# Performance work log

Measured on AMD Instinct MI355X. Metric: run time of the kernel, lower is better.

## Reference

```python
import jax, jax.numpy as jnp
import numpy as np

B, T, S, H = 4, 128, 512, 512
LN_EPS = 1e-5


def setup_inputs() -> dict:
    key = jax.random.key(0)
    ks = jax.random.split(key, 10)
    query = jax.random.normal(ks[0], (B, T, H), dtype=jnp.float32)
    encoder_outputs = jax.random.normal(ks[1], (B, S, H), dtype=jnp.float32)
    src_lengths = jax.random.randint(ks[2], (B,), 1, S + 1, dtype=jnp.int32)
    # Parameters (nn.Linear stores weight as (out, in); we apply x @ W.T)
    W_h = jax.random.normal(ks[3], (H, H), dtype=jnp.float32) / np.sqrt(H)
    W_s = jax.random.normal(ks[4], (H, H), dtype=jnp.float32) / np.sqrt(H)
    v = jax.random.normal(ks[5], (H,), dtype=jnp.float32) * 0.01
    W_out = jax.random.normal(ks[6], (H, 2 * H), dtype=jnp.float32) / np.sqrt(2 * H)
    b_out = jnp.zeros((H,), dtype=jnp.float32)
    gamma = jnp.ones((H,), dtype=jnp.float32)
    beta = jnp.zeros((H,), dtype=jnp.float32)
    return {
        "query": query, "encoder_outputs": encoder_outputs, "src_lengths": src_lengths,
        "W_h": W_h, "W_s": W_s, "v": v, "W_out": W_out, "b_out": b_out,
        "gamma": gamma, "beta": beta,
    }


def reference(query, encoder_outputs, src_lengths, W_h, W_s, v, W_out, b_out, gamma, beta):
    # Project query and encoder states: (b,t,h) and (b,s,h)
    q_proj = jnp.einsum('bth,oh->bto', query, W_s)
    k_proj = jnp.einsum('bsh,oh->bso', encoder_outputs, W_h)
    # Additive score: tanh over broadcast-add, then dot with v -> (b,t,s)
    score = jnp.einsum('btsh,h->bts', jnp.tanh(q_proj[:, :, None, :] + k_proj[:, None, :, :]), v)
    # Mask padded source positions (src_idx >= length)
    pad = jnp.arange(S)[None, :] >= src_lengths[:, None]          # (b,s)
    score = jnp.where(pad[:, None, :], -jnp.inf, score)
    attn = jax.nn.softmax(score, axis=-1)                          # (b,t,s)
    context = jnp.einsum('bts,bsh->bth', attn, encoder_outputs)    # (b,t,h)
    cq = jnp.concatenate([context, query], axis=-1)                # (b,t,2h)
    out = jnp.tanh(jnp.einsum('btk,ok->bto', cq, W_out) + b_out)
    # LayerNorm over last dim
    mu = jnp.mean(out, axis=-1, keepdims=True)
    var = jnp.mean(jnp.square(out - mu), axis=-1, keepdims=True)
    return (out - mu) / jnp.sqrt(var + LN_EPS) * gamma + beta
```

## Files before the change

kernel.cpp:

```cpp
#include <hip/hip_runtime.h>
#include <hip/hip_bf16.h>
#include <math.h>

#define B 4
#define T 128
#define S 512
#define H 512
#define QK_SCALE 2.8853900817779268f

#if defined(__has_builtin)
#if __has_builtin(__builtin_amdgcn_exp2f)
#define EXP2F(x) __builtin_amdgcn_exp2f(x)
#else
#define EXP2F(x) __expf((x) * 0.6931471805599453f)
#endif
#else
#define EXP2F(x) __expf((x) * 0.6931471805599453f)
#endif

typedef __attribute__((ext_vector_type(8))) short bf16x8;
typedef __attribute__((ext_vector_type(4))) float f32x4;

__device__ __forceinline__ short f2b(float x) {
    unsigned int u = __float_as_uint(x);
    u += 0x7fffu + ((u >> 16) & 1u);
    return (short)(u >> 16);
}
__device__ __forceinline__ float fast_tanh(float x) {
    float e = __expf(2.0f * x);
    float r = __builtin_amdgcn_rcpf(e + 1.0f);
    return 1.0f - 2.0f * r;
}

__global__ __launch_bounds__(256) void cvt_all(
    const float* __restrict__ q, const float* __restrict__ Ws,
    const float* __restrict__ Wh, const float* __restrict__ Wo,
    const float* __restrict__ enc, const int* __restrict__ slen,
    short* __restrict__ qb, short* __restrict__ wsb, short* __restrict__ whb,
    short* __restrict__ wob, short* __restrict__ eb, short* __restrict__ encT) {
    const int bid = blockIdx.x;
    const int tid = threadIdx.x;
    if (bid >= 1152) {
        __shared__ short tb[32][33];
        const int bid2 = bid - 1152;
        const int b = bid2 >> 8, s0 = ((bid2 >> 4) & 15) * 32, h0 = (bid2 & 15) * 32;
        if (s0 >= slen[b]) return;
        const int r = tid >> 3, c = (tid & 7) * 4;
        float4 a = *(const float4*)&enc[((size_t)(b * S + s0 + r)) * H + h0 + c];
        tb[c + 0][r] = f2b(a.x); tb[c + 1][r] = f2b(a.y);
        tb[c + 2][r] = f2b(a.z); tb[c + 3][r] = f2b(a.w);
        __syncthreads();
        ushort4 o = make_ushort4((unsigned short)tb[r][c], (unsigned short)tb[r][c + 1],
                                 (unsigned short)tb[r][c + 2], (unsigned short)tb[r][c + 3]);
        *(ushort4*)&encT[((size_t)(b * H + h0 + r)) * S + s0 + c] = o;
        return;
    }
    size_t i = ((size_t)bid * 256 + tid) * 8;
    const float* src; short* dst; size_t off;
    if (i < 262144)        { src = q;   dst = qb;  off = i; }
    else if (i < 524288)   { src = Ws;  dst = wsb; off = i - 262144; }
    else if (i < 786432)   { src = Wh;  dst = whb; off = i - 524288; }
    else if (i < 1310720)  { src = Wo;  dst = wob; off = i - 786432; }
    else                   { src = enc; dst = eb;  off = i - 1310720; }
    float4 a = *(const float4*)(src + off);
    float4 b = *(const float4*)(src + off + 4);
    ushort4 o0 = make_ushort4((unsigned short)f2b(a.x), (unsigned short)f2b(a.y),
                              (unsigned short)f2b(a.z), (unsigned short)f2b(a.w));
    ushort4 o1 = make_ushort4((unsigned short)f2b(b.x), (unsigned short)f2b(b.y),
                              (unsigned short)f2b(b.z), (unsigned short)f2b(b.w));
    *(ushort4*)(dst + off) = o0;
    *(ushort4*)(dst + off + 4) = o1;
}

#define MFMA4(APTR0, APTR1, BPTR0, BPTR1, KOFF)                                  \
    {                                                                            \
        bf16x8 a0 = *(const bf16x8*)((APTR0) + (KOFF));                          \
        bf16x8 a1 = *(const bf16x8*)((APTR1) + (KOFF));                          \
        bf16x8 b0 = *(const bf16x8*)((BPTR0) + (KOFF));                          \
        bf16x8 b1 = *(const bf16x8*)((BPTR1) + (KOFF));                          \
        acc00 = __builtin_amdgcn_mfma_f32_16x16x32_bf16(a0, b0, acc00, 0, 0, 0); \
        acc01 = __builtin_amdgcn_mfma_f32_16x16x32_bf16(a0, b1, acc01, 0, 0, 0); \
        acc10 = __builtin_amdgcn_mfma_f32_16x16x32_bf16(a1, b0, acc10, 0, 0, 0); \
        acc11 = __builtin_amdgcn_mfma_f32_16x16x32_bf16(a1, b1, acc11, 0, 0, 0); \
    }

__global__ __launch_bounds__(64) void mfma_proj(
    const short* __restrict__ qb, const short* __restrict__ eb,
    const short* __restrict__ wsb, const short* __restrict__ whb,
    const int* __restrict__ slen, float* __restrict__ qe, float* __restrict__ ke) {
    const int lane = threadIdx.x;
    const int r = lane & 15, kb = lane >> 4;
    const int n0 = blockIdx.x * 32;
    const int m0 = blockIdx.y * 32;
    const short* A; const short* W; float* C;
    if (m0 < 512) { A = qb + (size_t)m0 * H; W = wsb; C = qe + (size_t)m0 * H; }
    else {
        const int row = m0 - 512;
        if ((row & 511) >= slen[row >> 9]) return;
        A = eb + (size_t)row * H; W = whb; C = ke + (size_t)row * H;
    }
    const short* a0p = A + (size_t)r * H + kb * 8;
    const short* a1p = a0p + 16 * H;
    const short* b0p = W + (size_t)(n0 + r) * H + kb * 8;
    const short* b1p = b0p + 16 * H;
    f32x4 acc00 = {0,0,0,0}, acc01 = {0,0,0,0}, acc10 = {0,0,0,0}, acc11 = {0,0,0,0};
#pragma unroll 4
    for (int k = 0; k < H; k += 32) MFMA4(a0p, a1p, b0p, b1p, k)
    const int cr = kb * 4, cc = r;
#pragma unroll
    for (int g = 0; g < 4; ++g) {
        C[(size_t)(cr + g) * H + n0 + cc]           = EXP2F(acc00[g] * QK_SCALE);
        C[(size_t)(cr + g) * H + n0 + 16 + cc]      = EXP2F(acc01[g] * QK_SCALE);
        C[(size_t)(16 + cr + g) * H + n0 + cc]      = EXP2F(acc10[g] * QK_SCALE);
        C[(size_t)(16 + cr + g) * H + n0 + 16 + cc] = EXP2F(acc11[g] * QK_SCALE);
    }
}

__global__ __launch_bounds__(64) void score_v4(
    const float* __restrict__ qe, const float* __restrict__ ke,
    const float* __restrict__ v, const int* __restrict__ slen,
    float* __restrict__ scoreh) {
    const int qt = blockIdx.z & 3;
    const int b = blockIdx.z >> 2;
    const int L = slen[b];
    const int sbase = blockIdx.x * 16;
    if (sbase >= L) return;
    const int tbase = blockIdx.y * 8;
    const int hbase = qt * 128;
    __shared__ __align__(16) float qs[8][132];
    __shared__ __align__(16) float ks[16][132];
    __shared__ __align__(16) float vsh[128];
    const int lane = threadIdx.x;
    {
        const int r = lane >> 3, c = (lane & 7) * 16;
        const float* qsrc = qe + (size_t)(b * T + tbase + r) * H + hbase + c;
        const float* k0src = ke + (size_t)(b * S + sbase + r) * H + hbase + c;
        const float* k1src = k0src + 8 * H;
#pragma unroll
        for (int j = 0; j < 4; ++j) {
            *(float4*)&qs[r][c + j * 4] = *(const float4*)(qsrc + j * 4);
            *(float4*)&ks[r][c + j * 4] = *(const float4*)(k0src + j * 4);
            *(float4*)&ks[8 + r][c + j * 4] = *(const float4*)(k1src + j * 4);
        }
        float2 vv = *(const float2*)&v[hbase + lane * 2];
        *(float2*)&vsh[lane * 2] = make_float2(-2.f * vv.x, -2.f * vv.y);
    }
    __syncthreads();
    const int t = lane >> 3, s0 = (lane & 7) * 2;
    const float* qrow = &qs[t][0];
    const float* k0r = &ks[s0][0];
    const float* k1r = &ks[s0 + 1][0];
    float a0 = 0.f, a1 = 0.f, c0 = 0.f, c1 = 0.f;
#pragma unroll 2
    for (int i = 0; i < 128; i += 4) {
        float4 q4 = *(const float4*)&qrow[i];
        float4 ka = *(const float4*)&k0r[i];
        float4 kb = *(const float4*)&k1r[i];
        float4 v4 = *(const float4*)&vsh[i];
        a0 = fmaf(v4.x, __builtin_amdgcn_rcpf(fmaf(q4.x, ka.x, 1.f)), a0);
        c0 = fmaf(v4.x, __builtin_amdgcn_rcpf(fmaf(q4.x, kb.x, 1.f)), c0);
        a1 = fmaf(v4.y, __builtin_amdgcn_rcpf(fmaf(q4.y, ka.y, 1.f)), a1);
        c1 = fmaf(v4.y, __builtin_amdgcn_rcpf(fmaf(q4.y, kb.y, 1.f)), c1);
        a0 = fmaf(v4.z, __builtin_amdgcn_rcpf(fmaf(q4.z, ka.z, 1.f)), a0);
        c0 = fmaf(v4.z, __builtin_amdgcn_rcpf(fmaf(q4.z, kb.z, 1.f)), c0);
        a1 = fmaf(v4.w, __builtin_amdgcn_rcpf(fmaf(q4.w, ka.w, 1.f)), a1);
        c1 = fmaf(v4.w, __builtin_amdgcn_rcpf(fmaf(q4.w, kb.w, 1.f)), c1);
    }
    *(float2*)&scoreh[((size_t)qt * (B * T) + b * T + tbase + t) * S + sbase + s0] =
        make_float2(a0 + a1, c0 + c1);
}

__global__ __launch_bounds__(256) void softmax_k(
    const float* __restrict__ scoreh, const int* __restrict__ slen,
    short* __restrict__ attnb) {
    __shared__ float red[8];
    const int row = blockIdx.x;
    const int L = slen[row >> 7];
    const int tid = threadIdx.x;
    const int lane = tid & 63, wv = tid >> 6;
    const size_t sl = (size_t)(B * T) * S;
    const float* p0 = scoreh + (size_t)row * S;
    float x0 = p0[tid] + p0[sl + tid] + p0[2 * sl + tid] + p0[3 * sl + tid];
    float x1 = p0[tid + 256] + p0[sl + tid + 256] + p0[2 * sl + tid + 256] +
               p0[3 * sl + tid + 256];
    if (tid >= L) x0 = -INFINITY;
    if (tid + 256 >= L) x1 = -INFINITY;
    float m = fmaxf(x0, x1);
#pragma unroll
    for (int off = 32; off > 0; off >>= 1) m = fmaxf(m, __shfl_xor(m, off));
    if (lane == 0) red[wv] = m;
    __syncthreads();
    m = fmaxf(fmaxf(red[0], red[1]), fmaxf(red[2], red[3]));
    float e0 = __expf(x0 - m);
    float e1 = __expf(x1 - m);
    float sm = e0 + e1;
#pragma unroll
    for (int off = 32; off > 0; off >>= 1) sm += __shfl_xor(sm, off);
    if (lane == 0) red[4 + wv] = sm;
    __syncthreads();
    float inv = 1.0f / (red[4] + red[5] + red[6] + red[7]);
    short* o = attnb + (size_t)row * S;
    o[tid] = f2b(e0 * inv);
    o[tid + 256] = f2b(e1 * inv);
}

__global__ __launch_bounds__(64) void mfma_ctx(
    const short* __restrict__ attnb, const short* __restrict__ encT,
    const int* __restrict__ slen, short* __restrict__ ctxb) {
    const int b = blockIdx.z;
    const int L = slen[b];
    const int Keff = min(S, (L + 31) & ~31);
    const int lane = threadIdx.x;
    const int r = lane & 15, kb = lane >> 4;
    const int m0 = blockIdx.y * 32;
    const int n0 = blockIdx.x * 32;
    const short* A = attnb + (size_t)(b * T + m0) * S;
    const short* Bp = encT + (size_t)b * H * S;
    const short* a0p = A + (size_t)r * S + kb * 8;
    const short* a1p = a0p + 16 * S;
    const short* b0p = Bp + (size_t)(n0 + r) * S + kb * 8;
    const short* b1p = b0p + 16 * S;
    f32x4 acc00 = {0,0,0,0}, acc01 = {0,0,0,0}, acc10 = {0,0,0,0}, acc11 = {0,0,0,0};
#pragma unroll 2
    for (int k = 0; k < Keff; k += 32) MFMA4(a0p, a1p, b0p, b1p, k)
    const int cr = kb * 4, cc = r;
#pragma unroll
    for (int g = 0; g < 4; ++g) {
        size_t row0 = (size_t)(b * T + m0 + cr + g) * H;
        size_t row1 = (size_t)(b * T + m0 + 16 + cr + g) * H;
        ctxb[row0 + n0 + cc]      = f2b(acc00[g]);
        ctxb[row0 + n0 + 16 + cc] = f2b(acc01[g]);
        ctxb[row1 + n0 + cc]      = f2b(acc10[g]);
        ctxb[row1 + n0 + 16 + cc] = f2b(acc11[g]);
    }
}

__global__ __launch_bounds__(64) void mfma_out(
    const short* __restrict__ ctxb, const short* __restrict__ qb,
    const short* __restrict__ wob, const float* __restrict__ bias,
    float* __restrict__ pre) {
    const int lane = threadIdx.x;
    const int r = lane & 15, kb = lane >> 4;
    const int m0 = blockIdx.y * 32, n0 = blockIdx.x * 32;
    f32x4 acc00 = {0,0,0,0}, acc01 = {0,0,0,0}, acc10 = {0,0,0,0}, acc11 = {0,0,0,0};
    const short* b0p = wob + (size_t)(n0 + r) * (2 * H) + kb * 8;
    const short* b1p = b0p + 16 * (2 * H);
    {
        const short* a0p = ctxb + (size_t)(m0 + r) * H + kb * 8;
        const short* a1p = a0p + 16 * H;
#pragma unroll 4
        for (int k = 0; k < H; k += 32) MFMA4(a0p, a1p, b0p, b1p, k)
    }
    {
        const short* a0p = qb + (size_t)(m0 + r) * H + kb * 8;
        const short* a1p = a0p + 16 * H;
        const short* c0p = b0p + H;
        const short* c1p = b1p + H;
#pragma unroll 4
        for (int k = 0; k < H; k += 32) MFMA4(a0p, a1p, c0p, c1p, k)
    }
    const int cr = kb * 4, cc = r;
    float bn0 = bias[n0 + cc], bn1 = bias[n0 + 16 + cc];
#pragma unroll
    for (int g = 0; g < 4; ++g) {
        size_t row0 = (size_t)(m0 + cr + g) * H;
        size_t row1 = (size_t)(m0 + 16 + cr + g) * H;
        pre[row0 + n0 + cc]      = fast_tanh(acc00[g] + bn0);
        pre[row0 + n0 + 16 + cc] = fast_tanh(acc01[g] + bn1);
        pre[row1 + n0 + cc]      = fast_tanh(acc10[g] + bn0);
        pre[row1 + n0 + 16 + cc] = fast_tanh(acc11[g] + bn1);
    }
}

__global__ __launch_bounds__(256) void ln_out(
    const float* __restrict__ X, const float* __restrict__ gamma,
    const float* __restrict__ beta, float* __restrict__ out) {
    __shared__ float red[8];
    const int r = blockIdx.x;
    const int tid = threadIdx.x;
    const int lane = tid & 63, wv = tid >> 6;
    const float* x = X + (size_t)r * H;
    float x0 = x[tid], x1 = x[tid + 256];
    float s = x0 + x1;
#pragma unroll
    for (int off = 32; off > 0; off >>= 1) s += __shfl_down(s, off);
    if (lane == 0) red[wv] = s;
    __syncthreads();
    float mu = (red[0] + red[1] + red[2] + red[3]) * (1.0f / H);
    float d0 = x0 - mu, d1 = x1 - mu;
    float vsum = d0 * d0 + d1 * d1;
#pragma unroll
    for (int off = 32; off > 0; off >>= 1) vsum += __shfl_down(vsum, off);
    if (lane == 0) red[4 + wv] = vsum;
    __syncthreads();
    float var = (red[4] + red[5] + red[6] + red[7]) * (1.0f / H);
    float inv = rsqrtf(var + 1e-5f);
    out[(size_t)r * H + tid] = d0 * inv * gamma[tid] + beta[tid];
    out[(size_t)r * H + tid + 256] = d1 * inv * gamma[tid + 256] + beta[tid + 256];
}

extern "C" void kernel_launch(void* const* d_in, const int* in_sizes, int n_in,
                              void* d_out, int out_size, void* d_ws, size_t ws_size,
                              hipStream_t stream) {
    const float* query = (const float*)d_in[0];
    const float* enc   = (const float*)d_in[1];
    const int*   slen  = (const int*)d_in[2];
    const float* W_h   = (const float*)d_in[3];
    const float* W_s   = (const float*)d_in[4];
    const float* v     = (const float*)d_in[5];
    const float* W_out = (const float*)d_in[6];
    const float* b_out = (const float*)d_in[7];
    const float* gamma = (const float*)d_in[8];
    const float* beta  = (const float*)d_in[9];
    float* out = (float*)d_out;

    char* base = (char*)d_ws;
    short* qb     = (short*)(base + 0);
    short* wsb    = (short*)(base + 524288);
    short* whb    = (short*)(base + 1048576);
    short* wob    = (short*)(base + 1572864);
    short* eb     = (short*)(base + 2621440);
    float* qe     = (float*)(base + 4718592);
    float* ke     = (float*)(base + 5767168);
    float* scoreh = (float*)(base + 9961472);
    short* attnb  = (short*)(base + 14155776);
    short* encT   = (short*)(base + 14680064);
    short* ctxb   = (short*)(base + 16777216);
    float* pre    = (float*)(base + 17301504);

    cvt_all<<<dim3(2176), dim3(256), 0, stream>>>(query, W_s, W_h, W_out, enc, slen,
                                                  qb, wsb, whb, wob, eb, encT);
    mfma_proj<<<dim3(16, 80), dim3(64), 0, stream>>>(qb, eb, wsb, whb, slen, qe, ke);
    score_v4<<<dim3(32, 16, 16), dim3(64), 0, stream>>>(qe, ke, v, slen, scoreh);
    softmax_k<<<dim3(B * T), dim3(256), 0, stream>>>(scoreh, slen, attnb);
    mfma_ctx<<<dim3(16, 4, 4), dim3(64), 0, stream>>>(attnb, encT, slen, ctxb);
    mfma_out<<<dim3(16, 16), dim3(64), 0, stream>>>(ctxb, qb, wob, b_out, pre);
    ln_out<<<dim3(B * T), dim3(256), 0, stream>>>(pre, gamma, beta, out);
}
```

Baseline: 65.60 us.

## Fuse softmax, context GEMM, output GEMM and LayerNorm into one tail kernel

Replaces four launches (softmax, context MFMA, output MFMA, LayerNorm) with a single 1024-thread kernel per 16-row tile. Attention weights and context stay in shared memory, and LayerNorm statistics are reduced in-block with single-pass sum and sum-of-squares. This removes three launches and the global round trips for attn, ctx and pre. In exchange the tail runs on only 32 blocks, which limits parallelism, and each block re-reads the full W_out and encT slice. The context GEMM also drops the Keff length-based skip of padded positions.

```diff
diff --git a/kernel.cpp b/kernel.cpp
--- a/kernel.cpp
+++ b/kernel.cpp
@@ -170,133 +170,152 @@
         make_float2(a0 + a1, c0 + c1);
 }
 
-__global__ __launch_bounds__(256) void softmax_k(
+__global__ __launch_bounds__(1024) void tail_kernel(
     const float* __restrict__ scoreh, const int* __restrict__ slen,
-    short* __restrict__ attnb) {
-    __shared__ float red[8];
-    const int row = blockIdx.x;
-    const int L = slen[row >> 7];
+    const short* __restrict__ encT, const short* __restrict__ qb,
+    const short* __restrict__ wob, const float* __restrict__ bias,
+    const float* __restrict__ gamma, const float* __restrict__ beta,
+    float* __restrict__ out) {
+    __shared__ __align__(16) short attn_s[16][520];
+    __shared__ __align__(16) short ctx_s[16][520];
+    __shared__ float red_s[16][16];
+    __shared__ float red_q[16][16];
+    __shared__ float fin[16][2];
     const int tid = threadIdx.x;
-    const int lane = tid & 63, wv = tid >> 6;
-    const size_t sl = (size_t)(B * T) * S;
-    const float* p0 = scoreh + (size_t)row * S;
-    float x0 = p0[tid] + p0[sl + tid] + p0[2 * sl + tid] + p0[3 * sl + tid];
-    float x1 = p0[tid + 256] + p0[sl + tid + 256] + p0[2 * sl + tid + 256] +
-               p0[3 * sl + tid + 256];
-    if (tid >= L) x0 = -INFINITY;
-    if (tid + 256 >= L) x1 = -INFINITY;
-    float m = fmaxf(x0, x1);
-#pragma unroll
-    for (int off = 32; off > 0; off >>= 1) m = fmaxf(m, __shfl_xor(m, off));
-    if (lane == 0) red[wv] = m;
-    __syncthreads();
-    m = fmaxf(fmaxf(red[0], red[1]), fmaxf(red[2], red[3]));
-    float e0 = __expf(x0 - m);
-    float e1 = __expf(x1 - m);
-    float sm = e0 + e1;
-#pragma unroll
-    for (int off = 32; off > 0; off >>= 1) sm += __shfl_xor(sm, off);
-    if (lane == 0) red[4 + wv] = sm;
-    __syncthreads();
-    float inv = 1.0f / (red[4] + red[5] + red[6] + red[7]);
-    short* o = attnb + (size_t)row * S;
-    o[tid] = f2b(e0 * inv);
-    o[tid + 256] = f2b(e1 * inv);
-}
-
-__global__ __launch_bounds__(64) void mfma_ctx(
-    const short* __restrict__ attnb, const short* __restrict__ encT,
-    const int* __restrict__ slen, short* __restrict__ ctxb) {
-    const int b = blockIdx.z;
+    const int w = tid >> 6, lane = tid & 63;
+    const int b = blockIdx.x >> 3;
+    const int tb = (blockIdx.x & 7) * 16;
     const int L = slen[b];
-    const int Keff = min(S, (L + 31) & ~31);
-    const int lane = threadIdx.x;
+
+    {
+        const int grow = b * T + tb + w;
+        const size_t sl = (size_t)(B * T) * S;
+        const float* p = scoreh + (size_t)grow * S + lane * 8;
+        float x[8];
+#pragma unroll
+        for (int j = 0; j < 2; ++j) {
+            float4 q0 = *(const float4*)(p + j * 4);
+            float4 q1 = *(const float4*)(p + sl + j * 4);
+            float4 q2 = *(const float4*)(p + 2 * sl + j * 4);
+            float4 q3 = *(const float4*)(p + 3 * sl + j * 4);
+            x[j * 4 + 0] = q0.x + q1.x + q2.x + q3.x;
+            x[j * 4 + 1] = q0.y + q1.y + q2.y + q3.y;
+            x[j * 4 + 2] = q0.z + q1.z + q2.z + q3.z;
+            x[j * 4 + 3] = q0.w + q1.w + q2.w + q3.w;
+        }
+        const int cbase = lane * 8;
+#pragma unroll
+        for (int j = 0; j < 8; ++j)
+            if (cbase + j >= L) x[j] = -INFINITY;
+        float m = x[0];
+#pragma unroll
+        for (int j = 1; j < 8; ++j) m = fmaxf(m, x[j]);
+#pragma unroll
+        for (int off = 1; off < 64; off <<= 1) m = fmaxf(m, __shfl_xor(m, off));
+        float e[8], sm = 0.f;
+#pragma unroll
+        for (int j = 0; j < 8; ++j) { e[j] = __expf(x[j] - m); sm += e[j]; }
+#pragma unroll
+        for (int off = 1; off < 64; off <<= 1) sm += __shfl_xor(sm, off);
+        float inv = 1.0f / sm;
+        ushort4 u0 = make_ushort4((unsigned short)f2b(e[0] * inv), (unsigned short)f2b(e[1] * inv),
+                                  (unsigned short)f2b(e[2] * inv), (unsigned short)f2b(e[3] * inv));
+        ushort4 u1 = make_ushort4((unsigned short)f2b(e[4] * inv), (unsigned short)f2b(e[5] * inv),
+                                  (unsigned short)f2b(e[6] * inv), (unsigned short)f2b(e[7] * inv));
+        *(ushort4*)&attn_s[w][lane * 8]     = u0;
+        *(ushort4*)&attn_s[w][lane * 8 + 4] = u1;
+    }
+    __syncthreads();
+
     const int r = lane & 15, kb = lane >> 4;
-    const int m0 = blockIdx.y * 32;
-    const int n0 = blockIdx.x * 32;
-    const short* A = attnb + (size_t)(b * T + m0) * S;
-    const short* Bp = encT + (size_t)b * H * S;
-    const short* a0p = A + (size_t)r * S + kb * 8;
-    const short* a1p = a0p + 16 * S;
-    const short* b0p = Bp + (size_t)(n0 + r) * S + kb * 8;
-    const short* b1p = b0p + 16 * S;
-    f32x4 acc00 = {0,0,0,0}, acc01 = {0,0,0,0}, acc10 = {0,0,0,0}, acc11 = {0,0,0,0};
-#pragma unroll 2
-    for (int k = 0; k < Keff; k += 32) MFMA4(a0p, a1p, b0p, b1p, k)
-    const int cr = kb * 4, cc = r;
+    const int n0 = w * 32;
+    {
+        f32x4 cc0 = {0,0,0,0}, cc1 = {0,0,0,0};
+        const short* bp0 = encT + ((size_t)(b * H + n0 + r)) * S + kb * 8;
+        const short* bp1 = bp0 + (size_t)16 * S;
+#pragma unroll 4
+        for (int k = 0; k < S; k += 32) {
+            bf16x8 a = *(const bf16x8*)&attn_s[r][k + kb * 8];
+            cc0 = __builtin_amdgcn_mfma_f32_16x16x32_bf16(a, *(const bf16x8*)(bp0 + k), cc0, 0, 0, 0);
+            cc1 = __builtin_amdgcn_mfma_f32_16x16x32_bf16(a, *(const bf16x8*)(bp1 + k), cc1, 0, 0, 0);
+        }
+        const int cr = kb * 4;
+#pragma unroll
+        for (int g = 0; g < 4; ++g) {
+            ctx_s[cr + g][n0 + r]      = f2b(cc0[g]);
+            ctx_s[cr + g][n0 + 16 + r] = f2b(cc1[g]);
+        }
+    }
+    __syncthreads();
+
+    f32x4 o0 = {0,0,0,0}, o1 = {0,0,0,0};
+    {
+        const short* w0p = wob + ((size_t)(n0 + r)) * (2 * H) + kb * 8;
+        const short* w1p = w0p + (size_t)16 * (2 * H);
+#pragma unroll 4
+        for (int k = 0; k < H; k += 32) {
+            bf16x8 a = *(const bf16x8*)&ctx_s[r][k + kb * 8];
+            o0 = __builtin_amdgcn_mfma_f32_16x16x32_bf16(a, *(const bf16x8*)(w0p + k), o0, 0, 0, 0);
+            o1 = __builtin_amdgcn_mfma_f32_16x16x32_bf16(a, *(const bf16x8*)(w1p + k), o1, 0, 0, 0);
+        }
+        const short* qp = qb + ((size_t)(b * T + tb + r)) * H + kb * 8;
+#pragma unroll 4
+        for (int k = 0; k < H; k += 32) {
+            bf16x8 a = *(const bf16x8*)(qp + k);
+            o0 = __builtin_amdgcn_mfma_f32_16x16x32_bf16(a, *(const bf16x8*)(w0p + H + k), o0, 0, 0, 0);
+            o1 = __builtin_amdgcn_mfma_f32_16x16x32_bf16(a, *(const bf16x8*)(w1p + H + k), o1, 0, 0, 0);
+        }
+    }
+    const int cr = kb * 4;
+    float bn0 = bias[n0 + r], bn1 = bias[n0 + 16 + r];
+    float v0[4], v1[4], sA[4], sQ[4];
 #pragma unroll
     for (int g = 0; g < 4; ++g) {
-        size_t row0 = (size_t)(b * T + m0 + cr + g) * H;
-        size_t row1 = (size_t)(b * T + m0 + 16 + cr + g) * H;
-        ctxb[row0 + n0 + cc]      = f2b(acc00[g]);
-        ctxb[row0 + n0 + 16 + cc] = f2b(acc01[g]);
-        ctxb[row1 + n0 + cc]      = f2b(acc10[g]);
-        ctxb[row1 + n0 + 16 + cc] = f2b(acc11[g]);
-    }
-}
-
-__global__ __launch_bounds__(64) void mfma_out(
-    const short* __restrict__ ctxb, const short* __restrict__ qb,
-    const short* __restrict__ wob, const float* __restrict__ bias,
-    float* __restrict__ pre) {
-    const int lane = threadIdx.x;
-    const int r = lane & 15, kb = lane >> 4;
-    const int m0 = blockIdx.y * 32, n0 = blockIdx.x * 32;
-    f32x4 acc00 = {0,0,0,0}, acc01 = {0,0,0,0}, acc10 = {0,0,0,0}, acc11 = {0,0,0,0};
-    const short* b0p = wob + (size_t)(n0 + r) * (2 * H) + kb * 8;
-    const short* b1p = b0p + 16 * (2 * H);
-    {
-        const short* a0p = ctxb + (size_t)(m0 + r) * H + kb * 8;
-        const short* a1p = a0p + 16 * H;
-#pragma unroll 4
-        for (int k = 0; k < H; k += 32) MFMA4(a0p, a1p, b0p, b1p, k)
-    }
-    {
-        const short* a0p = qb + (size_t)(m0 + r) * H + kb * 8;
-        const short* a1p = a0p + 16 * H;
-        const short* c0p = b0p + H;
-        const short* c1p = b1p + H;
-#pragma unroll 4
-        for (int k = 0; k < H; k += 32) MFMA4(a0p, a1p, c0p, c1p, k)
-    }
-    const int cr = kb * 4, cc = r;
-    float bn0 = bias[n0 + cc], bn1 = bias[n0 + 16 + cc];
+        v0[g] = fast_tanh(o0[g] + bn0);
+        v1[g] = fast_tanh(o1[g] + bn1);
+        sA[g] = v0[g] + v1[g];
+        sQ[g] = v0[g] * v0[g] + v1[g] * v1[g];
+    }
+#pragma unroll
+    for (int off = 1; off < 16; off <<= 1) {
+#pragma unroll
+        for (int g = 0; g < 4; ++g) {
+            sA[g] += __shfl_xor(sA[g], off);
+            sQ[g] += __shfl_xor(sQ[g], off);
+        }
+    }
+    if (r == 0) {
+#pragma unroll
+        for (int g = 0; g < 4; ++g) {
+            red_s[cr + g][w] = sA[g];
+            red_q[cr + g][w] = sQ[g];
+        }
+    }
+    __syncthreads();
+    if (lane < 16) {
+        float ts = red_s[w][lane], tq = red_q[w][lane];
+#pragma unroll
+        for (int off = 1; off < 16; off <<= 1) {
+            ts += __shfl_xor(ts, off);
+            tq += __shfl_xor(tq, off);
+        }
+        if (lane == 0) {
+            float mu = ts * (1.0f / H);
+            float var = tq * (1.0f / H) - mu * mu;
+            fin[w][0] = mu;
+            fin[w][1] = rsqrtf(var + 1e-5f);
+        }
+    }
+    __syncthreads();
 #pragma unroll
     for (int g = 0; g < 4; ++g) {
-        size_t row0 = (size_t)(m0 + cr + g) * H;
-        size_t row1 = (size_t)(m0 + 16 + cr + g) * H;
-        pre[row0 + n0 + cc]      = fast_tanh(acc00[g] + bn0);
-        pre[row0 + n0 + 16 + cc] = fast_tanh(acc01[g] + bn1);
-        pre[row1 + n0 + cc]      = fast_tanh(acc10[g] + bn0);
-        pre[row1 + n0 + 16 + cc] = fast_tanh(acc11[g] + bn1);
-    }
-}
-
-__global__ __launch_bounds__(256) void ln_out(
-    const float* __restrict__ X, const float* __restrict__ gamma,
-    const float* __restrict__ beta, float* __restrict__ out) {
-    __shared__ float red[8];
-    const int r = blockIdx.x;
-    const int tid = threadIdx.x;
-    const int lane = tid & 63, wv = tid >> 6;
-    const float* x = X + (size_t)r * H;
-    float x0 = x[tid], x1 = x[tid + 256];
-    float s = x0 + x1;
-#pragma unroll
-    for (int off = 32; off > 0; off >>= 1) s += __shfl_down(s, off);
-    if (lane == 0) red[wv] = s;
-    __syncthreads();
-    float mu = (red[0] + red[1] + red[2] + red[3]) * (1.0f / H);
-    float d0 = x0 - mu, d1 = x1 - mu;
-    float vsum = d0 * d0 + d1 * d1;
-#pragma unroll
-    for (int off = 32; off > 0; off >>= 1) vsum += __shfl_down(vsum, off);
-    if (lane == 0) red[4 + wv] = vsum;
-    __syncthreads();
-    float var = (red[4] + red[5] + red[6] + red[7]) * (1.0f / H);
-    float inv = rsqrtf(var + 1e-5f);
-    out[(size_t)r * H + tid] = d0 * inv * gamma[tid] + beta[tid];
-    out[(size_t)r * H + tid + 256] = d1 * inv * gamma[tid + 256] + beta[tid + 256];
+        const int row = cr + g;
+        const float mu = fin[row][0], inv = fin[row][1];
+        const int col0 = n0 + r, col1 = n0 + 16 + r;
+        const size_t orow = (size_t)(b * T + tb + row) * H;
+        out[orow + col0] = (v0[g] - mu) * inv * gamma[col0] + beta[col0];
+        out[orow + col1] = (v1[g] - mu) * inv * gamma[col1] + beta[col1];
+    }
 }
 
 extern "C" void kernel_launch(void* const* d_in, const int* in_sizes, int n_in,
@@ -323,17 +342,12 @@
     float* qe     = (float*)(base + 4718592);
     float* ke     = (float*)(base + 5767168);
     float* scoreh = (float*)(base + 9961472);
-    short* attnb  = (short*)(base + 14155776);
-    short* encT   = (short*)(base + 14680064);
-    short* ctxb   = (short*)(base + 16777216);
-    float* pre    = (float*)(base + 17301504);
+    short* encT   = (short*)(base + 14155776);
 
     cvt_all<<<dim3(2176), dim3(256), 0, stream>>>(query, W_s, W_h, W_out, enc, slen,
                                                   qb, wsb, whb, wob, eb, encT);
     mfma_proj<<<dim3(16, 80), dim3(64), 0, stream>>>(qb, eb, wsb, whb, slen, qe, ke);
     score_v4<<<dim3(32, 16, 16), dim3(64), 0, stream>>>(qe, ke, v, slen, scoreh);
-    softmax_k<<<dim3(B * T), dim3(256), 0, stream>>>(scoreh, slen, attnb);
-    mfma_ctx<<<dim3(16, 4, 4), dim3(64), 0, stream>>>(attnb, encT, slen, ctxb);
-    mfma_out<<<dim3(16, 16), dim3(64), 0, stream>>>(ctxb, qb, wob, b_out, pre);
-    ln_out<<<dim3(B * T), dim3(256), 0, stream>>>(pre, gamma, beta, out);
-}
+    tail_kernel<<<dim3(32), dim3(1024), 0, stream>>>(scoreh, slen, encT, qb, wob,
+                                                     b_out, gamma, beta, out);
+}
```

Result: slower. 99.34 us (+51.4%).

## Reassociate output projection through attention and drop separate softmax and context GEMM

Applied to the files above, without the earlier changes.

The context path is reassociated: the encoder outputs are projected through the context half of W_out inside a merged projection kernel. The query half of W_out is also precomputed there, so the final GEMM multiplies unnormalized exp-scores directly by the projected encoder values and applies the 1/Z normalization in the epilogue. Softmax becomes a lighter combine kernel with no max subtraction, and the separate context GEMM and encoder transpose are removed, cutting launches and intermediate traffic. In exchange the encoder-side projection does about four times the FLOPs of the old context GEMM. Skipping the max-shift relies on scores staying bounded, which risks overflow for larger v.

```diff
diff --git a/kernel.cpp b/kernel.cpp
--- a/kernel.cpp
+++ b/kernel.cpp
@@ -35,27 +35,10 @@
 __global__ __launch_bounds__(256) void cvt_all(
     const float* __restrict__ q, const float* __restrict__ Ws,
     const float* __restrict__ Wh, const float* __restrict__ Wo,
-    const float* __restrict__ enc, const int* __restrict__ slen,
+    const float* __restrict__ enc,
     short* __restrict__ qb, short* __restrict__ wsb, short* __restrict__ whb,
-    short* __restrict__ wob, short* __restrict__ eb, short* __restrict__ encT) {
-    const int bid = blockIdx.x;
-    const int tid = threadIdx.x;
-    if (bid >= 1152) {
-        __shared__ short tb[32][33];
-        const int bid2 = bid - 1152;
-        const int b = bid2 >> 8, s0 = ((bid2 >> 4) & 15) * 32, h0 = (bid2 & 15) * 32;
-        if (s0 >= slen[b]) return;
-        const int r = tid >> 3, c = (tid & 7) * 4;
-        float4 a = *(const float4*)&enc[((size_t)(b * S + s0 + r)) * H + h0 + c];
-        tb[c + 0][r] = f2b(a.x); tb[c + 1][r] = f2b(a.y);
-        tb[c + 2][r] = f2b(a.z); tb[c + 3][r] = f2b(a.w);
-        __syncthreads();
-        ushort4 o = make_ushort4((unsigned short)tb[r][c], (unsigned short)tb[r][c + 1],
-                                 (unsigned short)tb[r][c + 2], (unsigned short)tb[r][c + 3]);
-        *(ushort4*)&encT[((size_t)(b * H + h0 + r)) * S + s0 + c] = o;
-        return;
-    }
-    size_t i = ((size_t)bid * 256 + tid) * 8;
+    short* __restrict__ wob, short* __restrict__ eb) {
+    size_t i = ((size_t)blockIdx.x * 256 + threadIdx.x) * 8;
     const float* src; short* dst; size_t off;
     if (i < 262144)        { src = q;   dst = qb;  off = i; }
     else if (i < 524288)   { src = Ws;  dst = wsb; off = i - 262144; }
@@ -72,47 +55,88 @@
     *(ushort4*)(dst + off + 4) = o1;
 }
 
-#define MFMA4(APTR0, APTR1, BPTR0, BPTR1, KOFF)                                  \
-    {                                                                            \
-        bf16x8 a0 = *(const bf16x8*)((APTR0) + (KOFF));                          \
-        bf16x8 a1 = *(const bf16x8*)((APTR1) + (KOFF));                          \
-        bf16x8 b0 = *(const bf16x8*)((BPTR0) + (KOFF));                          \
-        bf16x8 b1 = *(const bf16x8*)((BPTR1) + (KOFF));                          \
-        acc00 = __builtin_amdgcn_mfma_f32_16x16x32_bf16(a0, b0, acc00, 0, 0, 0); \
-        acc01 = __builtin_amdgcn_mfma_f32_16x16x32_bf16(a0, b1, acc01, 0, 0, 0); \
-        acc10 = __builtin_amdgcn_mfma_f32_16x16x32_bf16(a1, b0, acc10, 0, 0, 0); \
-        acc11 = __builtin_amdgcn_mfma_f32_16x16x32_bf16(a1, b1, acc11, 0, 0, 0); \
-    }
-
-__global__ __launch_bounds__(64) void mfma_proj(
+__global__ __launch_bounds__(64) void proj_mega(
     const short* __restrict__ qb, const short* __restrict__ eb,
     const short* __restrict__ wsb, const short* __restrict__ whb,
-    const int* __restrict__ slen, float* __restrict__ qe, float* __restrict__ ke) {
+    const short* __restrict__ wob, const int* __restrict__ slen,
+    float* __restrict__ qe, float* __restrict__ ke,
+    short* __restrict__ ewt, float* __restrict__ qw) {
+    const int job = blockIdx.x;
     const int lane = threadIdx.x;
     const int r = lane & 15, kb = lane >> 4;
-    const int n0 = blockIdx.x * 32;
-    const int m0 = blockIdx.y * 32;
-    const short* A; const short* W; float* C;
-    if (m0 < 512) { A = qb + (size_t)m0 * H; W = wsb; C = qe + (size_t)m0 * H; }
-    else {
-        const int row = m0 - 512;
-        if ((row & 511) >= slen[row >> 9]) return;
-        A = eb + (size_t)row * H; W = whb; C = ke + (size_t)row * H;
-    }
-    const short* a0p = A + (size_t)r * H + kb * 8;
-    const short* a1p = a0p + 16 * H;
-    const short* b0p = W + (size_t)(n0 + r) * H + kb * 8;
-    const short* b1p = b0p + 16 * H;
+    const short* A; int lda;
+    const short* W; int ldw;
+    int epi;
+    float* Cf = nullptr; short* Cb = nullptr; int ldc;
+    if (job < 256) {
+        const int m0 = (job >> 4) * 32, n0 = (job & 15) * 32;
+        A = qb + (size_t)m0 * H; lda = H;
+        W = wsb + (size_t)n0 * H; ldw = H;
+        Cf = qe + (size_t)m0 * H + n0; ldc = H; epi = 0;
+    } else if (job < 1280) {
+        const int j = job - 256;
+        const int m0 = (j >> 4) * 32, n0 = (j & 15) * 32;
+        if ((m0 & 511) >= slen[m0 >> 9]) return;
+        A = eb + (size_t)m0 * H; lda = H;
+        W = whb + (size_t)n0 * H; ldw = H;
+        Cf = ke + (size_t)m0 * H + n0; ldc = H; epi = 0;
+    } else if (job < 2304) {
+        const int j = job - 1280;
+        const int b = j >> 8;
+        const int m0 = ((j >> 4) & 15) * 32;
+        const int n0 = (j & 15) * 32;
+        if (n0 >= slen[b]) return;
+        A = wob + (size_t)m0 * (2 * H); lda = 2 * H;
+        W = eb + ((size_t)b * S + n0) * H; ldw = H;
+        Cb = ewt + (size_t)b * H * S + (size_t)m0 * S + n0; ldc = S; epi = 1;
+    } else {
+        const int j = job - 2304;
+        const int m0 = (j >> 4) * 32, n0 = (j & 15) * 32;
+        A = qb + (size_t)m0 * H; lda = H;
+        W = wob + (size_t)n0 * (2 * H) + H; ldw = 2 * H;
+        Cf = qw + (size_t)m0 * H + n0; ldc = H; epi = 2;
+    }
+    const short* a0p = A + (size_t)r * lda + kb * 8;
+    const short* a1p = a0p + (size_t)16 * lda;
+    const short* b0p = W + (size_t)r * ldw + kb * 8;
+    const short* b1p = b0p + (size_t)16 * ldw;
     f32x4 acc00 = {0,0,0,0}, acc01 = {0,0,0,0}, acc10 = {0,0,0,0}, acc11 = {0,0,0,0};
 #pragma unroll 4
-    for (int k = 0; k < H; k += 32) MFMA4(a0p, a1p, b0p, b1p, k)
+    for (int k = 0; k < H; k += 32) {
+        bf16x8 a0 = *(const bf16x8*)(a0p + k);
+        bf16x8 a1 = *(const bf16x8*)(a1p + k);
+        bf16x8 b0 = *(const bf16x8*)(b0p + k);
+        bf16x8 b1 = *(const bf16x8*)(b1p + k);
+        acc00 = __builtin_amdgcn_mfma_f32_16x16x32_bf16(a0, b0, acc00, 0, 0, 0);
+        acc01 = __builtin_amdgcn_mfma_f32_16x16x32_bf16(a0, b1, acc01, 0, 0, 0);
+        acc10 = __builtin_amdgcn_mfma_f32_16x16x32_bf16(a1, b0, acc10, 0, 0, 0);
+        acc11 = __builtin_amdgcn_mfma_f32_16x16x32_bf16(a1, b1, acc11, 0, 0, 0);
+    }
     const int cr = kb * 4, cc = r;
-#pragma unroll
-    for (int g = 0; g < 4; ++g) {
-        C[(size_t)(cr + g) * H + n0 + cc]           = EXP2F(acc00[g] * QK_SCALE);
-        C[(size_t)(cr + g) * H + n0 + 16 + cc]      = EXP2F(acc01[g] * QK_SCALE);
-        C[(size_t)(16 + cr + g) * H + n0 + cc]      = EXP2F(acc10[g] * QK_SCALE);
-        C[(size_t)(16 + cr + g) * H + n0 + 16 + cc] = EXP2F(acc11[g] * QK_SCALE);
+    if (epi == 0) {
+#pragma unroll
+        for (int g = 0; g < 4; ++g) {
+            Cf[(size_t)(cr + g) * ldc + cc]           = EXP2F(acc00[g] * QK_SCALE);
+            Cf[(size_t)(cr + g) * ldc + 16 + cc]      = EXP2F(acc01[g] * QK_SCALE);
+            Cf[(size_t)(16 + cr + g) * ldc + cc]      = EXP2F(acc10[g] * QK_SCALE);
+            Cf[(size_t)(16 + cr + g) * ldc + 16 + cc] = EXP2F(acc11[g] * QK_SCALE);
+        }
+    } else if (epi == 1) {
+#pragma unroll
+        for (int g = 0; g < 4; ++g) {
+            Cb[(size_t)(cr + g) * ldc + cc]           = f2b(acc00[g]);
+            Cb[(size_t)(cr + g) * ldc + 16 + cc]      = f2b(acc01[g]);
+            Cb[(size_t)(16 + cr + g) * ldc + cc]      = f2b(acc10[g]);
+            Cb[(size_t)(16 + cr + g) * ldc + 16 + cc] = f2b(acc11[g]);
+        }
+    } else {
+#pragma unroll
+        for (int g = 0; g < 4; ++g) {
+            Cf[(size_t)(cr + g) * ldc + cc]           = acc00[g];
+            Cf[(size_t)(cr + g) * ldc + 16 + cc]      = acc01[g];
+            Cf[(size_t)(16 + cr + g) * ldc + cc]      = acc10[g];
+            Cf[(size_t)(16 + cr + g) * ldc + 16 + cc] = acc11[g];
+        }
     }
 }
 
@@ -170,105 +194,89 @@
         make_float2(a0 + a1, c0 + c1);
 }
 
-__global__ __launch_bounds__(256) void softmax_k(
+__global__ __launch_bounds__(256) void combine_k(
     const float* __restrict__ scoreh, const int* __restrict__ slen,
-    short* __restrict__ attnb) {
-    __shared__ float red[8];
-    const int row = blockIdx.x;
+    short* __restrict__ U, float* __restrict__ Z) {
+    const int row = blockIdx.x * 4 + (threadIdx.x >> 6);
+    const int lane = threadIdx.x & 63;
     const int L = slen[row >> 7];
-    const int tid = threadIdx.x;
-    const int lane = tid & 63, wv = tid >> 6;
     const size_t sl = (size_t)(B * T) * S;
-    const float* p0 = scoreh + (size_t)row * S;
-    float x0 = p0[tid] + p0[sl + tid] + p0[2 * sl + tid] + p0[3 * sl + tid];
-    float x1 = p0[tid + 256] + p0[sl + tid + 256] + p0[2 * sl + tid + 256] +
-               p0[3 * sl + tid + 256];
-    if (tid >= L) x0 = -INFINITY;
-    if (tid + 256 >= L) x1 = -INFINITY;
-    float m = fmaxf(x0, x1);
-#pragma unroll
-    for (int off = 32; off > 0; off >>= 1) m = fmaxf(m, __shfl_xor(m, off));
-    if (lane == 0) red[wv] = m;
-    __syncthreads();
-    m = fmaxf(fmaxf(red[0], red[1]), fmaxf(red[2], red[3]));
-    float e0 = __expf(x0 - m);
-    float e1 = __expf(x1 - m);
-    float sm = e0 + e1;
-#pragma unroll
-    for (int off = 32; off > 0; off >>= 1) sm += __shfl_xor(sm, off);
-    if (lane == 0) red[4 + wv] = sm;
-    __syncthreads();
-    float inv = 1.0f / (red[4] + red[5] + red[6] + red[7]);
-    short* o = attnb + (size_t)row * S;
-    o[tid] = f2b(e0 * inv);
-    o[tid + 256] = f2b(e1 * inv);
-}
-
-__global__ __launch_bounds__(64) void mfma_ctx(
-    const short* __restrict__ attnb, const short* __restrict__ encT,
-    const int* __restrict__ slen, short* __restrict__ ctxb) {
-    const int b = blockIdx.z;
-    const int L = slen[b];
-    const int Keff = min(S, (L + 31) & ~31);
+    const float* p = scoreh + (size_t)row * S + lane * 8;
+    float e[8];
+    float sm = 0.f;
+#pragma unroll
+    for (int j = 0; j < 2; ++j) {
+        float4 q0 = *(const float4*)(p + j * 4);
+        float4 q1 = *(const float4*)(p + sl + j * 4);
+        float4 q2 = *(const float4*)(p + 2 * sl + j * 4);
+        float4 q3 = *(const float4*)(p + 3 * sl + j * 4);
+        e[j * 4 + 0] = __expf(q0.x + q1.x + q2.x + q3.x);
+        e[j * 4 + 1] = __expf(q0.y + q1.y + q2.y + q3.y);
+        e[j * 4 + 2] = __expf(q0.z + q1.z + q2.z + q3.z);
+        e[j * 4 + 3] = __expf(q0.w + q1.w + q2.w + q3.w);
+    }
+    const int cbase = lane * 8;
+#pragma unroll
+    for (int j = 0; j < 8; ++j) {
+        if (cbase + j >= L) e[j] = 0.f;
+        sm += e[j];
+    }
+#pragma unroll
+    for (int off = 1; off < 64; off <<= 1) sm += __shfl_xor(sm, off);
+    if (lane == 0) Z[row] = sm;
+    short* o = U + (size_t)row * S + cbase;
+    ushort4 u0 = make_ushort4((unsigned short)f2b(e[0]), (unsigned short)f2b(e[1]),
+                              (unsigned short)f2b(e[2]), (unsigned short)f2b(e[3]));
+    ushort4 u1 = make_ushort4((unsigned short)f2b(e[4]), (unsigned short)f2b(e[5]),
+                              (unsigned short)f2b(e[6]), (unsigned short)f2b(e[7]));
+    *(ushort4*)o = u0;
+    *(ushort4*)(o + 4) = u1;
+}
+
+__global__ __launch_bounds__(64) void mfma_out2(
+    const short* __restrict__ U, const short* __restrict__ ewt,
+    const float* __restrict__ qw, const float* __restrict__ Z,
+    const int* __restrict__ slen, const float* __restrict__ bias,
+    float* __restrict__ pre) {
     const int lane = threadIdx.x;
     const int r = lane & 15, kb = lane >> 4;
     const int m0 = blockIdx.y * 32;
     const int n0 = blockIdx.x * 32;
-    const short* A = attnb + (size_t)(b * T + m0) * S;
-    const short* Bp = encT + (size_t)b * H * S;
+    const int b = m0 >> 7;
+    const int L = slen[b];
+    const int Keff = min(S, (L + 31) & ~31);
+    const short* A = U + (size_t)m0 * S;
+    const short* Bp = ewt + (size_t)b * H * S;
     const short* a0p = A + (size_t)r * S + kb * 8;
     const short* a1p = a0p + 16 * S;
     const short* b0p = Bp + (size_t)(n0 + r) * S + kb * 8;
     const short* b1p = b0p + 16 * S;
     f32x4 acc00 = {0,0,0,0}, acc01 = {0,0,0,0}, acc10 = {0,0,0,0}, acc11 = {0,0,0,0};
 #pragma unroll 2
-    for (int k = 0; k < Keff; k += 32) MFMA4(a0p, a1p, b0p, b1p, k)
-    const int cr = kb * 4, cc = r;
-#pragma unroll
-    for (int g = 0; g < 4; ++g) {
-        size_t row0 = (size_t)(b * T + m0 + cr + g) * H;
-        size_t row1 = (size_t)(b * T + m0 + 16 + cr + g) * H;
-        ctxb[row0 + n0 + cc]      = f2b(acc00[g]);
-        ctxb[row0 + n0 + 16 + cc] = f2b(acc01[g]);
-        ctxb[row1 + n0 + cc]      = f2b(acc10[g]);
-        ctxb[row1 + n0 + 16 + cc] = f2b(acc11[g]);
-    }
-}
-
-__global__ __launch_bounds__(64) void mfma_out(
-    const short* __restrict__ ctxb, const short* __restrict__ qb,
-    const short* __restrict__ wob, const float* __restrict__ bias,
-    float* __restrict__ pre) {
-    const int lane = threadIdx.x;
-    const int r = lane & 15, kb = lane >> 4;
-    const int m0 = blockIdx.y * 32, n0 = blockIdx.x * 32;
-    f32x4 acc00 = {0,0,0,0}, acc01 = {0,0,0,0}, acc10 = {0,0,0,0}, acc11 = {0,0,0,0};
-    const short* b0p = wob + (size_t)(n0 + r) * (2 * H) + kb * 8;
-    const short* b1p = b0p + 16 * (2 * H);
-    {
-        const short* a0p = ctxb + (size_t)(m0 + r) * H + kb * 8;
-        const short* a1p = a0p + 16 * H;
-#pragma unroll 4
-        for (int k = 0; k < H; k += 32) MFMA4(a0p, a1p, b0p, b1p, k)
-    }
-    {
-        const short* a0p = qb + (size_t)(m0 + r) * H + kb * 8;
-        const short* a1p = a0p + 16 * H;
-        const short* c0p = b0p + H;
-        const short* c1p = b1p + H;
-#pragma unroll 4
-        for (int k = 0; k < H; k += 32) MFMA4(a0p, a1p, c0p, c1p, k)
+    for (int k = 0; k < Keff; k += 32) {
+        bf16x8 a0 = *(const bf16x8*)(a0p + k);
+        bf16x8 a1 = *(const bf16x8*)(a1p + k);
+        bf16x8 b0 = *(const bf16x8*)(b0p + k);
+        bf16x8 b1 = *(const bf16x8*)(b1p + k);
+        acc00 = __builtin_amdgcn_mfma_f32_16x16x32_bf16(a0, b0, acc00, 0, 0, 0);
+        acc01 = __builtin_amdgcn_mfma_f32_16x16x32_bf16(a0, b1, acc01, 0, 0, 0);
+        acc10 = __builtin_amdgcn_mfma_f32_16x16x32_bf16(a1, b0, acc10, 0, 0, 0);
+        acc11 = __builtin_amdgcn_mfma_f32_16x16x32_bf16(a1, b1, acc11, 0, 0, 0);
     }
     const int cr = kb * 4, cc = r;
     float bn0 = bias[n0 + cc], bn1 = bias[n0 + 16 + cc];
 #pragma unroll
     for (int g = 0; g < 4; ++g) {
-        size_t row0 = (size_t)(m0 + cr + g) * H;
-        size_t row1 = (size_t)(m0 + 16 + cr + g) * H;
-        pre[row0 + n0 + cc]      = fast_tanh(acc00[g] + bn0);
-        pre[row0 + n0 + 16 + cc] = fast_tanh(acc01[g] + bn1);
-        pre[row1 + n0 + cc]      = fast_tanh(acc10[g] + bn0);
-        pre[row1 + n0 + 16 + cc] = fast_tanh(acc11[g] + bn1);
+        const int gr0 = m0 + cr + g;
+        const int gr1 = gr0 + 16;
+        float iz0 = __builtin_amdgcn_rcpf(Z[gr0]);
+        float iz1 = __builtin_amdgcn_rcpf(Z[gr1]);
+        size_t row0 = (size_t)gr0 * H;
+        size_t row1 = (size_t)gr1 * H;
+        pre[row0 + n0 + cc]      = fast_tanh(fmaf(acc00[g], iz0, qw[row0 + n0 + cc]) + bn0);
+        pre[row0 + n0 + 16 + cc] = fast_tanh(fmaf(acc01[g], iz0, qw[row0 + n0 + 16 + cc]) + bn1);
+        pre[row1 + n0 + cc]      = fast_tanh(fmaf(acc10[g], iz1, qw[row1 + n0 + cc]) + bn0);
+        pre[row1 + n0 + 16 + cc] = fast_tanh(fmaf(acc11[g], iz1, qw[row1 + n0 + 16 + cc]) + bn1);
     }
 }
 
@@ -315,25 +323,26 @@
     float* out = (float*)d_out;
 
     char* base = (char*)d_ws;
-    short* qb     = (short*)(base + 0);
-    short* wsb    = (short*)(base + 524288);
-    short* whb    = (short*)(base + 1048576);
-    short* wob    = (short*)(base + 1572864);
-    short* eb     = (short*)(base + 2621440);
-    float* qe     = (float*)(base + 4718592);
-    float* ke     = (float*)(base + 5767168);
-    float* scoreh = (float*)(base + 9961472);
-    short* attnb  = (short*)(base + 14155776);
-    short* encT   = (short*)(base + 14680064);
-    short* ctxb   = (short*)(base + 16777216);
-    float* pre    = (float*)(base + 17301504);
-
-    cvt_all<<<dim3(2176), dim3(256), 0, stream>>>(query, W_s, W_h, W_out, enc, slen,
-                                                  qb, wsb, whb, wob, eb, encT);
-    mfma_proj<<<dim3(16, 80), dim3(64), 0, stream>>>(qb, eb, wsb, whb, slen, qe, ke);
+    short* qb     = (short*)(base + 0x000000);
+    short* wsb    = (short*)(base + 0x080000);
+    short* whb    = (short*)(base + 0x100000);
+    short* wob    = (short*)(base + 0x180000);
+    short* eb     = (short*)(base + 0x280000);
+    float* qe     = (float*)(base + 0x480000);
+    float* ke     = (float*)(base + 0x580000);
+    float* scoreh = (float*)(base + 0x980000);
+    short* U      = (short*)(base + 0xD80000);
+    short* ewt    = (short*)(base + 0xE00000);
+    float* qw     = (float*)(base + 0x1000000);
+    float* Z      = (float*)(base + 0x1100000);
+    float* pre    = (float*)(base + 0x1101000);
+
+    cvt_all<<<dim3(1152), dim3(256), 0, stream>>>(query, W_s, W_h, W_out, enc,
+                                                  qb, wsb, whb, wob, eb);
+    proj_mega<<<dim3(2560), dim3(64), 0, stream>>>(qb, eb, wsb, whb, wob, slen,
+                                                   qe, ke, ewt, qw);
     score_v4<<<dim3(32, 16, 16), dim3(64), 0, stream>>>(qe, ke, v, slen, scoreh);
-    softmax_k<<<dim3(B * T), dim3(256), 0, stream>>>(scoreh, slen, attnb);
-    mfma_ctx<<<dim3(16, 4, 4), dim3(64), 0, stream>>>(attnb, encT, slen, ctxb);
-    mfma_out<<<dim3(16, 16), dim3(64), 0, stream>>>(ctxb, qb, wob, b_out, pre);
+    combine_k<<<dim3(128), dim3(256), 0, stream>>>(scoreh, slen, U, Z);
+    mfma_out2<<<dim3(16, 16), dim3(64), 0, stream>>>(U, ewt, qw, Z, slen, b_out, pre);
     ln_out<<<dim3(B * T), dim3(256), 0, stream>>>(pre, gamma, beta, out);
 }
```

Measured after the change: 65.16 us. Within noise of the previous version (-0.7%).
